# Kernel optimization log

Measured on AMD Instinct MI355X. Metric: run time of the kernel, lower is better.

Reference implementation:

```python
import jax, jax.numpy as jnp
import numpy as np

B, D, K = 131072, 64, 4096

def setup_inputs() -> dict:
    key = jax.random.key(0)
    k1, k2 = jax.random.split(key)
    z_e = jax.random.normal(k1, (B, D), dtype=jnp.float32)
    # nn.init.uniform_(-1/K, 1/K)
    codebook = jax.random.uniform(k2, (K, D), dtype=jnp.float32, minval=-1.0 / K, maxval=1.0 / K)
    return {"z_e": z_e, "codebook": codebook}

def reference(z_e, codebook):
    # squared-distance expansion: ||z||^2 + ||e||^2 - 2 z.e  -> (B, K)
    z2 = jnp.sum(z_e * z_e, axis=1, keepdims=True)          # (B, 1)
    e2 = jnp.sum(codebook * codebook, axis=1)[None, :]       # (1, K)
    ze = jnp.einsum('bd,kd->bk', z_e, codebook)              # (B, K)
    dist = z2 + e2 - 2.0 * ze
    codes = jnp.argmin(dist, axis=1)                         # (B,) int
    z_q = codebook[codes]                                    # (B, D) gather
    return (z_q, codes)
```

## Files before the change

### kernel.cpp

```cpp
#include <hip/hip_runtime.h>
#include <math.h>
#include <stdint.h>

#define Bn 131072
#define Dn 64
#define Kn 4096
#define TK 64
#define NKT (Kn / TK)
#define TPR 4
#define NRD (NKT / TPR)

typedef _Float16 f16x8 __attribute__((ext_vector_type(8)));
typedef float f32x4 __attribute__((ext_vector_type(4)));

__device__ __forceinline__ unsigned umn(unsigned a, unsigned b) { return a < b ? a : b; }
__device__ __forceinline__ unsigned umx(unsigned a, unsigned b) { return a > b ? a : b; }
__device__ __forceinline__ unsigned umed3(unsigned a, unsigned b, unsigned c) {
  unsigned d;
  asm("v_med3_u32 %0, %1, %2, %3" : "=v"(d) : "v"(a), "v"(b), "v"(c));
  return d;
}
__device__ __forceinline__ unsigned umn3(unsigned a, unsigned b, unsigned c) {
  return umn(umn(a, b), c);
}

__device__ __forceinline__ void stage16(const void* g, void* l) {
  __builtin_amdgcn_global_load_lds((const __attribute__((address_space(1))) unsigned int*)g,
                                   (__attribute__((address_space(3))) unsigned int*)l,
                                   16, 0, 0);
}

__global__ __launch_bounds__(256) void cvt_cb(const float* __restrict__ cb,
                                              unsigned char* __restrict__ img) {
  int u = blockIdx.x * 256 + threadIdx.x;
  int g = u >> 3;
  int p = u & 7;
  int kt = g >> 6;
  int n = g & 63;
  const float4* s = (const float4*)(cb + (size_t)g * Dn + p * 8);
  float4 c0 = s[0], c1 = s[1];
  f16x8 h;
  h[0] = (_Float16)(c0.x * 4096.f); h[1] = (_Float16)(c0.y * 4096.f);
  h[2] = (_Float16)(c0.z * 4096.f); h[3] = (_Float16)(c0.w * 4096.f);
  h[4] = (_Float16)(c1.x * 4096.f); h[5] = (_Float16)(c1.y * 4096.f);
  h[6] = (_Float16)(c1.z * 4096.f); h[7] = (_Float16)(c1.w * 4096.f);
  *(f16x8*)(img + (size_t)kt * 8192 + n * 128 + ((p ^ (n & 7)) << 4)) = h;
}

__global__ __launch_bounds__(512, 4) void vq_main(const float* __restrict__ z,
                                                  const float* __restrict__ cb,
                                                  const unsigned char* __restrict__ img,
                                                  float* __restrict__ out) {
  __shared__ __align__(16) unsigned char smem[66560];
  unsigned char* bufA = smem;
  unsigned char* bufB = smem + 32768;
  const int tid = threadIdx.x;
  const int lane = tid & 63;
  const int w = tid >> 6;
  const int q = lane >> 4;
  const int col = lane & 15;
  const int row0 = blockIdx.x * 256;

  const unsigned char* wsrc = img + tid * 16;
#pragma unroll
  for (int j = 0; j < TPR; ++j)
    stage16(wsrc + (size_t)j * 8192, bufA + j * 8192 + tid * 16);

  f16x8 A[2][2];
#pragma unroll
  for (int i = 0; i < 2; ++i)
#pragma unroll
    for (int c = 0; c < 2; ++c) {
      const float* zp = z + (size_t)(row0 + w * 32 + i * 16 + col) * Dn + c * 32 + q * 8;
      float4 x0 = *(const float4*)zp;
      float4 x1 = *(const float4*)(zp + 4);
      f16x8 a;
      a[0] = (_Float16)(-2.f * x0.x); a[1] = (_Float16)(-2.f * x0.y);
      a[2] = (_Float16)(-2.f * x0.z); a[3] = (_Float16)(-2.f * x0.w);
      a[4] = (_Float16)(-2.f * x1.x); a[5] = (_Float16)(-2.f * x1.y);
      a[6] = (_Float16)(-2.f * x1.z); a[7] = (_Float16)(-2.f * x1.w);
      A[i][c] = a;
    }

  f32x4 acc[2][4];
  unsigned k1[2][4], k2[2][4];
#pragma unroll
  for (int i = 0; i < 2; ++i)
#pragma unroll
    for (int r = 0; r < 4; ++r) { k1[i][r] = 0xFFFFFFFFu; k2[i][r] = 0xFFFFFFFFu; }
  unsigned tg[4] = {0u << 6, 1u << 6, 2u << 6, 3u << 6};
  const f32x4 c256 = {256.f, 256.f, 256.f, 256.f};

  for (int rd = 0; rd < NRD; ++rd) {
    unsigned char* bcur = (rd & 1) ? bufB : bufA;
    unsigned char* bnxt = (rd & 1) ? bufA : bufB;
    asm volatile("s_waitcnt vmcnt(0)" ::: "memory");
    __builtin_amdgcn_s_barrier();
    __builtin_amdgcn_sched_barrier(0);
    if (rd + 1 < NRD) {
#pragma unroll
      for (int j = 0; j < TPR; ++j)
        stage16(wsrc + ((size_t)(rd + 1) * TPR + j) * 8192, bnxt + j * 8192 + tid * 16);
    }

#pragma unroll
    for (int j = 0; j < TPR; ++j) {
      const unsigned char* tb = bcur + j * 8192;
#pragma unroll
      for (int c = 0; c < 2; ++c)
#pragma unroll
        for (int t = 0; t < 4; ++t) {
          f16x8 Bf = *(const f16x8*)(tb + (t * 16 + col) * 128 + (((c * 4 + q) ^ (col & 7)) << 4));
#pragma unroll
          for (int i = 0; i < 2; ++i)
            acc[i][t] = __builtin_amdgcn_mfma_f32_16x16x32_f16(A[i][c], Bf,
                                                               (c == 0) ? c256 : acc[i][t], 0, 0, 0);
        }

#pragma unroll
      for (int i = 0; i < 2; ++i)
#pragma unroll
        for (int r = 0; r < 4; ++r) {
          unsigned K0 = (__float_as_uint(acc[i][0][r]) & 0xFFFFFF00u) | tg[0];
          unsigned K1v = (__float_as_uint(acc[i][1][r]) & 0xFFFFFF00u) | tg[1];
          unsigned K2v = (__float_as_uint(acc[i][2][r]) & 0xFFFFFF00u) | tg[2];
          unsigned K3v = (__float_as_uint(acc[i][3][r]) & 0xFFFFFF00u) | tg[3];
          unsigned s1 = umn(K0, K1v), s2 = umx(K0, K1v);
          unsigned s3 = umn(K2v, K3v), s4 = umx(K2v, K3v);
          unsigned m3 = umed3(k1[i][r], s1, s3);
          unsigned n3 = umn3(k2[i][r], s2, s4);
          k1[i][r] = umn3(k1[i][r], s1, s3);
          k2[i][r] = umn(m3, n3);
        }
#pragma unroll
      for (int t = 0; t < 4; ++t) tg[t] += 1;
    }
  }

  __syncthreads();
  unsigned* dmp = (unsigned*)smem;
#pragma unroll
  for (int i = 0; i < 2; ++i)
#pragma unroll
    for (int r = 0; r < 4; ++r) {
      int rb = w * 32 + i * 16 + q * 4 + r;
      dmp[rb * 33 + col * 2] = k1[i][r];
      dmp[rb * 33 + col * 2 + 1] = k2[i][r];
    }
  __syncthreads();

  {
    const int rl = tid >> 1;
    const int half = tid & 1;
    const unsigned* keys = dmp + rl * 33 + half * 16;
    unsigned mk = 0xFFFFFFFFu;
    for (int j = 0; j < 16; ++j) mk = umn(mk, keys[j]);
    const float lim = __uint_as_float(mk & 0xFFFFFF00u) + 0.5f;

    const float4* zr4 = (const float4*)(z + (size_t)(row0 + rl) * Dn);

    float r8[8];
#pragma unroll
    for (int g = 0; g < 2; ++g) {
      float4 v = zr4[g]; int j = g * 4;
      r8[j + 0] = __fmul_rn(v.x, v.x); r8[j + 1] = __fmul_rn(v.y, v.y);
      r8[j + 2] = __fmul_rn(v.z, v.z); r8[j + 3] = __fmul_rn(v.w, v.w);
    }
#pragma unroll
    for (int g = 2; g < 16; ++g) {
      float4 v = zr4[g]; int j = (g & 1) * 4;
      r8[j + 0] = __fadd_rn(r8[j + 0], __fmul_rn(v.x, v.x));
      r8[j + 1] = __fadd_rn(r8[j + 1], __fmul_rn(v.y, v.y));
      r8[j + 2] = __fadd_rn(r8[j + 2], __fmul_rn(v.z, v.z));
      r8[j + 3] = __fadd_rn(r8[j + 3], __fmul_rn(v.w, v.w));
    }
    float z2f = __fadd_rn(__fadd_rn(__fadd_rn(r8[0], r8[1]), __fadd_rn(r8[2], r8[3])),
                          __fadd_rn(__fadd_rn(r8[4], r8[5]), __fadd_rn(r8[6], r8[7])));

    float bq = INFINITY; int bc = Kn;
    for (int j = 0; j < 16; ++j) {
      unsigned key = keys[j];
      float sc = __uint_as_float(key & 0xFFFFFF00u);
      if (sc > lim) continue;
      int c2 = half * 16 + j;
      int tag = (int)(key & 0xFFu);
      int code = (tag & 63) * 64 + (tag >> 6) * 16 + (c2 >> 1);
      const float4* cr = (const float4*)(cb + (size_t)code * Dn);
      double ze = 0.0;
      float e8[8];
#pragma unroll
      for (int g = 0; g < 16; ++g) {
        float4 ev = cr[g]; float4 zv = zr4[g];
        ze += (double)ev.x * (double)zv.x + (double)ev.y * (double)zv.y +
              (double)ev.z * (double)zv.z + (double)ev.w * (double)zv.w;
        int jj = (g & 1) * 4;
        if (g < 2) {
          e8[jj + 0] = __fmul_rn(ev.x, ev.x); e8[jj + 1] = __fmul_rn(ev.y, ev.y);
          e8[jj + 2] = __fmul_rn(ev.z, ev.z); e8[jj + 3] = __fmul_rn(ev.w, ev.w);
        } else {
          e8[jj + 0] = __fadd_rn(e8[jj + 0], __fmul_rn(ev.x, ev.x));
          e8[jj + 1] = __fadd_rn(e8[jj + 1], __fmul_rn(ev.y, ev.y));
          e8[jj + 2] = __fadd_rn(e8[jj + 2], __fmul_rn(ev.z, ev.z));
          e8[jj + 3] = __fadd_rn(e8[jj + 3], __fmul_rn(ev.w, ev.w));
        }
      }
      float e2f = __fadd_rn(__fadd_rn(__fadd_rn(e8[0], e8[1]), __fadd_rn(e8[2], e8[3])),
                            __fadd_rn(__fadd_rn(e8[4], e8[5]), __fadd_rn(e8[6], e8[7])));
      float zef = (float)ze;
      float t1 = __fadd_rn(z2f, e2f);
      float t2 = __fmul_rn(2.0f, zef);
      float qv = __fadd_rn(t1, -t2);
      if (qv < bq || (qv == bq && code < bc)) { bq = qv; bc = code; }
    }
    float obq = __shfl_xor(bq, 1);
    int obc = __shfl_xor(bc, 1);
    if (obq < bq || (obq == bq && obc < bc)) { bq = obq; bc = obc; }
    if (half == 0) {
      ((int*)(smem + 65536))[rl] = bc;
      out[(size_t)Bn * Dn + row0 + rl] = (float)bc;
    }
  }
  __syncthreads();

  {
    const float4* cb4 = (const float4*)cb;
    float4* out4 = (float4*)out;
    const int* wc = (const int*)(smem + 65536);
#pragma unroll
    for (int i = 0; i < 8; ++i) {
      int t = i * 512 + tid;
      int r = t >> 4, c2 = t & 15;
      int wn = wc[r];
      out4[(size_t)(row0 + r) * 16 + c2] = cb4[(size_t)wn * 16 + c2];
    }
  }
}

extern "C" void kernel_launch(void* const* d_in, const int* in_sizes, int n_in,
                              void* d_out, int out_size, void* d_ws, size_t ws_size,
                              hipStream_t stream) {
  const float* z = (const float*)d_in[0];
  const float* cb = (const float*)d_in[1];
  float* out = (float*)d_out;
  unsigned char* img = (unsigned char*)d_ws;
  cvt_cb<<<128, 256, 0, stream>>>(cb, img);
  vq_main<<<Bn / 256, 512, 0, stream>>>(z, cb, img, out);
}
```

Measured before the change: 205.4 us.

## Interleave MFMA and top-2 update per tile column; relax occupancy bound

Restructures the inner loop so that each 16-column codebook sub-tile's MFMAs are immediately followed by a streaming top-2 update with med3/min, instead of accumulating all four sub-tiles first and then running a batched sort network. This cuts live accumulator registers and lets the scalar comparisons interleave with matrix work. It also wraps the MFMAs in s_setprio and lowers the launch-bounds occupancy hint from 4 to 2 waves-per-EU blocks, giving the compiler more register room. The streaming update uses more comparison instructions per key than the batched network, and the lower occupancy hint may reduce latency hiding.

```diff
diff --git a/kernel.cpp b/kernel.cpp
--- a/kernel.cpp
+++ b/kernel.cpp
@@ -14,14 +14,10 @@
 typedef float f32x4 __attribute__((ext_vector_type(4)));
 
 __device__ __forceinline__ unsigned umn(unsigned a, unsigned b) { return a < b ? a : b; }
-__device__ __forceinline__ unsigned umx(unsigned a, unsigned b) { return a > b ? a : b; }
 __device__ __forceinline__ unsigned umed3(unsigned a, unsigned b, unsigned c) {
   unsigned d;
   asm("v_med3_u32 %0, %1, %2, %3" : "=v"(d) : "v"(a), "v"(b), "v"(c));
   return d;
-}
-__device__ __forceinline__ unsigned umn3(unsigned a, unsigned b, unsigned c) {
-  return umn(umn(a, b), c);
 }
 
 __device__ __forceinline__ void stage16(const void* g, void* l) {
@@ -47,7 +43,7 @@
   *(f16x8*)(img + (size_t)kt * 8192 + n * 128 + ((p ^ (n & 7)) << 4)) = h;
 }
 
-__global__ __launch_bounds__(512, 4) void vq_main(const float* __restrict__ z,
+__global__ __launch_bounds__(512, 2) void vq_main(const float* __restrict__ z,
                                                   const float* __restrict__ cb,
                                                   const unsigned char* __restrict__ img,
                                                   float* __restrict__ out) {
@@ -82,7 +78,6 @@
       A[i][c] = a;
     }
 
-  f32x4 acc[2][4];
   unsigned k1[2][4], k2[2][4];
 #pragma unroll
   for (int i = 0; i < 2; ++i)
@@ -90,6 +85,7 @@
     for (int r = 0; r < 4; ++r) { k1[i][r] = 0xFFFFFFFFu; k2[i][r] = 0xFFFFFFFFu; }
   unsigned tg[4] = {0u << 6, 1u << 6, 2u << 6, 3u << 6};
   const f32x4 c256 = {256.f, 256.f, 256.f, 256.f};
+  const int xu = (col & 7) << 4;
 
   for (int rd = 0; rd < NRD; ++rd) {
     unsigned char* bcur = (rd & 1) ? bufB : bufA;
@@ -107,31 +103,27 @@
     for (int j = 0; j < TPR; ++j) {
       const unsigned char* tb = bcur + j * 8192;
 #pragma unroll
-      for (int c = 0; c < 2; ++c)
-#pragma unroll
-        for (int t = 0; t < 4; ++t) {
-          f16x8 Bf = *(const f16x8*)(tb + (t * 16 + col) * 128 + (((c * 4 + q) ^ (col & 7)) << 4));
-#pragma unroll
-          for (int i = 0; i < 2; ++i)
-            acc[i][t] = __builtin_amdgcn_mfma_f32_16x16x32_f16(A[i][c], Bf,
-                                                               (c == 0) ? c256 : acc[i][t], 0, 0, 0);
+      for (int t = 0; t < 4; ++t) {
+        const int rowb = (t * 16 + col) * 128;
+        f16x8 B0 = *(const f16x8*)(tb + rowb + ((q << 4) ^ xu));
+        f16x8 B1 = *(const f16x8*)(tb + rowb + (((4 + q) << 4) ^ xu));
+        __builtin_amdgcn_s_setprio(1);
+        f32x4 a0 = __builtin_amdgcn_mfma_f32_16x16x32_f16(A[0][0], B0, c256, 0, 0, 0);
+        f32x4 a1 = __builtin_amdgcn_mfma_f32_16x16x32_f16(A[1][0], B0, c256, 0, 0, 0);
+        a0 = __builtin_amdgcn_mfma_f32_16x16x32_f16(A[0][1], B1, a0, 0, 0, 0);
+        a1 = __builtin_amdgcn_mfma_f32_16x16x32_f16(A[1][1], B1, a1, 0, 0, 0);
+        __builtin_amdgcn_s_setprio(0);
+        const unsigned tgv = tg[t];
+#pragma unroll
+        for (int r = 0; r < 4; ++r) {
+          unsigned key0 = (__float_as_uint(a0[r]) & 0xFFFFFF00u) | tgv;
+          k2[0][r] = umed3(k1[0][r], k2[0][r], key0);
+          k1[0][r] = umn(k1[0][r], key0);
+          unsigned key1 = (__float_as_uint(a1[r]) & 0xFFFFFF00u) | tgv;
+          k2[1][r] = umed3(k1[1][r], k2[1][r], key1);
+          k1[1][r] = umn(k1[1][r], key1);
         }
-
-#pragma unroll
-      for (int i = 0; i < 2; ++i)
-#pragma unroll
-        for (int r = 0; r < 4; ++r) {
-          unsigned K0 = (__float_as_uint(acc[i][0][r]) & 0xFFFFFF00u) | tg[0];
-          unsigned K1v = (__float_as_uint(acc[i][1][r]) & 0xFFFFFF00u) | tg[1];
-          unsigned K2v = (__float_as_uint(acc[i][2][r]) & 0xFFFFFF00u) | tg[2];
-          unsigned K3v = (__float_as_uint(acc[i][3][r]) & 0xFFFFFF00u) | tg[3];
-          unsigned s1 = umn(K0, K1v), s2 = umx(K0, K1v);
-          unsigned s3 = umn(K2v, K3v), s4 = umx(K2v, K3v);
-          unsigned m3 = umed3(k1[i][r], s1, s3);
-          unsigned n3 = umn3(k2[i][r], s2, s4);
-          k1[i][r] = umn3(k1[i][r], s1, s3);
-          k2[i][r] = umn(m3, n3);
-        }
+      }
 #pragma unroll
       for (int t = 0; t < 4; ++t) tg[t] += 1;
     }
```

After: 223.2 us. +8.7%, slower.
